# Performance work log

Hardware: AMD Instinct MI355X
Metric: run time of the kernel (lower is better)

## Reference

```python
import jax, jax.numpy as jnp
import numpy as np

N_NODES = 100000
N_EDGES = 1600000
D_FEAT = 256


def _glorot(key, shape):
    fan_in = shape[0]
    return jax.random.normal(key, shape, jnp.float32) * (1.0 / np.sqrt(fan_in))


def setup_inputs() -> dict:
    key = jax.random.key(0)
    ks = jax.random.split(key, 8)
    return {
        "x": jax.random.normal(ks[0], (N_NODES, D_FEAT), jnp.float32),
        "edge_index": jax.random.randint(ks[1], (2, N_EDGES), 0, N_NODES, jnp.int32),
        "w1": _glorot(ks[2], (D_FEAT, 64)),
        "b1": jnp.zeros((64,), jnp.float32),
        "w2": _glorot(ks[3], (64, 32)),
        "b2": jnp.zeros((32,), jnp.float32),
        "wf1": _glorot(ks[4], (32, 16)),
        "bf1": jnp.zeros((16,), jnp.float32),
        "wf2": _glorot(ks[5], (16, 1)),
        "bf2": jnp.zeros((1,), jnp.float32),
    }


def reference(x, edge_index, w1, b1, w2, b2, wf1, bf1, wf2, bf2):
    n = x.shape[0]
    # GCNConv: add self-loops, symmetric D^{-1/2}(A+I)D^{-1/2} normalization
    loops = jnp.arange(n, dtype=edge_index.dtype)
    src = jnp.concatenate([edge_index[0], loops])  # message sources
    dst = jnp.concatenate([edge_index[1], loops])  # aggregation targets
    deg = jax.ops.segment_sum(jnp.ones_like(dst, x.dtype), dst, num_segments=n)
    dinv = jnp.where(deg > 0, jax.lax.rsqrt(jnp.maximum(deg, 1.0)), 0.0)
    norm = dinv[src] * dinv[dst]  # [E+N]

    def gcn_conv(h, W, b):
        hw = h @ W                                   # dense transform first (smaller msg dim)
        msg = hw[src] * norm[:, None]                # gather + scale
        return jax.ops.segment_sum(msg, dst, num_segments=n) + b  # scatter-add

    h = jax.nn.relu(gcn_conv(x, w1, b1))
    h = jax.nn.relu(gcn_conv(h, w2, b2))
    h = jax.nn.relu(h @ wf1 + bf1)
    out = h @ wf2 + bf2
    return out.squeeze(-1)  # [N]
```

## Files before the change

kernel.cpp:

```cpp
#include <hip/hip_runtime.h>
#include <cstdint>
#include <cstddef>

#define N_NODES 100000
#define N_EDGES 1600000

#define NBK   391
#define NPB   256
#define EPB   ((N_EDGES + NPB - 1) / NPB)
#define NSLOT (NBK * NPB)
#define NSB   ((NSLOT + 1023) / 1024)
#define ES_CAP (N_EDGES + NBK * 2048 + 64)

typedef __attribute__((ext_vector_type(8))) short bf16x8;
typedef __attribute__((ext_vector_type(4))) float f32x4;

__device__ __forceinline__ float b2f(unsigned short u) {
    return __uint_as_float(((unsigned)u) << 16);
}
__device__ __forceinline__ unsigned short f2b(float f) {
    unsigned x = __float_as_uint(f);
    return (unsigned short)((x + 0x7FFFu + ((x >> 16) & 1u)) >> 16);
}

__device__ __forceinline__ void split8a(const float* f, bf16x8& hi, bf16x8& lo) {
#pragma unroll
    for (int j = 0; j < 8; ++j) {
        unsigned u = __float_as_uint(f[j]);
        hi[j] = (short)(u >> 16);
        float l = f[j] - __uint_as_float(u & 0xFFFF0000u);
        lo[j] = (short)(__float_as_uint(l) >> 16);
    }
}
__device__ __forceinline__ void split8(const float4& a0, const float4& a1,
                                       bf16x8& hi, bf16x8& lo) {
    float f[8] = {a0.x, a0.y, a0.z, a0.w, a1.x, a1.y, a1.z, a1.w};
    split8a(f, hi, lo);
}


__global__ __launch_bounds__(256) void k_hist(const int* __restrict__ dst,
                                              int* __restrict__ gcnt,
                                              unsigned short* __restrict__ hwb1,
                                              unsigned short* __restrict__ hwb2, int E) {
    __shared__ int lh[NBK];
    int t = threadIdx.x, bid = blockIdx.x;
    if (bid == 0) {
        if (t < 64) hwb1[(size_t)N_NODES * 64 + t] = 0;
        else if (t < 96) hwb2[(size_t)N_NODES * 32 + (t - 64)] = 0;
    }
    for (int i = t; i < NBK; i += 256) lh[i] = 0;
    __syncthreads();
    int e0 = bid * EPB, e1 = min(E, e0 + EPB);
    for (int e = e0 + t; e < e1; e += 256) atomicAdd(&lh[dst[e] >> 8], 1);
    __syncthreads();
    for (int b = t; b < NBK; b += 256) gcnt[b * NPB + bid] = lh[b];
}

__global__ __launch_bounds__(1024) void k_scanA(int* __restrict__ g,
                                                int* __restrict__ bsum, int ntot) {
    __shared__ int s[1024];
    int t = threadIdx.x;
    int i = blockIdx.x * 1024 + t;
    int v = (i < ntot) ? g[i] : 0;
    s[t] = v;
    __syncthreads();
    for (int o = 1; o < 1024; o <<= 1) {
        int a = (t >= o) ? s[t - o] : 0;
        __syncthreads();
        s[t] += a;
        __syncthreads();
    }
    if (i < ntot) g[i] = s[t] - v;
    if (t == 1023) bsum[blockIdx.x] = s[1023];
}

__global__ __launch_bounds__(1024) void k_scanC(int* __restrict__ g,
                                                const int* __restrict__ bsum, int ntot) {
    __shared__ int sp[1024];
    int t = threadIdx.x;
    sp[t] = (t < blockIdx.x && t < NSB) ? bsum[t] : 0;
    __syncthreads();
    for (int o = 512; o > 0; o >>= 1) {
        if (t < o) sp[t] += sp[t + o];
        __syncthreads();
    }
    int pref = sp[0];
    int i = blockIdx.x * 1024 + t;
    if (i < ntot) g[i] += pref;
}

__global__ __launch_bounds__(256) void k_partition(const int* __restrict__ src,
                                                   const int* __restrict__ dst,
                                                   const int* __restrict__ base,
                                                   unsigned* __restrict__ ebuf, int E) {
    __shared__ int lcur[NBK];
    int t = threadIdx.x, bid = blockIdx.x;
    for (int b = t; b < NBK; b += 256) lcur[b] = base[b * NPB + bid];
    __syncthreads();
    int e0 = bid * EPB, e1 = min(E, e0 + EPB);
    for (int e = e0 + t; e < e1; e += 256) {
        int d = dst[e];
        int b = d >> 8;
        int p = atomicAdd(&lcur[b], 1);
        ebuf[p] = (unsigned)src[e] | ((unsigned)(d & 255) << 20);
    }
}

__global__ __launch_bounds__(256) void k_bucket_csr(const int* __restrict__ base,
                                                    const unsigned* __restrict__ ebuf,
                                                    int* __restrict__ cnt,
                                                    float* __restrict__ dinv,
                                                    int* __restrict__ off,
                                                    int* __restrict__ es, int n) {
    __shared__ int lc[256];
    __shared__ int ss[256];
    __shared__ int lo[256];
    __shared__ int lcur[256];
    int b = blockIdx.x, t = threadIdx.x;
    int rstart = base[b * NPB];
    int rend = (b == NBK - 1) ? N_EDGES : base[(b + 1) * NPB];
    int wstart = ((rstart + 7) & ~7) + b * 2048;
    lc[t] = 0;
    __syncthreads();
    for (int e = rstart + t; e < rend; e += 256) atomicAdd(&lc[(int)(ebuf[e] >> 20)], 1);
    __syncthreads();
    int v = lc[t];
    int vp = (v + 7) & ~7;
    ss[t] = vp;
    __syncthreads();
    for (int o = 1; o < 256; o <<= 1) {
        int a = (t >= o) ? ss[t - o] : 0;
        __syncthreads();
        ss[t] += a;
        __syncthreads();
    }
    lo[t] = ss[t] - vp;
    lcur[t] = 0;
    int node = b * 256 + t;
    if (node < n) {
        cnt[node] = vp;
        dinv[node] = rsqrtf((float)v + 1.0f);
        off[node] = wstart + lo[t];
    }
    __syncthreads();
    for (int e = rstart + t; e < rend; e += 256) {
        unsigned u = ebuf[e];
        int l = (int)(u >> 20);
        int p = atomicAdd(&lcur[l], 1);
        es[wstart + lo[l] + p] = (int)(u & 0xFFFFFu);
    }
    for (int q = v; q < vp; ++q) es[wstart + lo[t] + q] = N_NODES;
}


__global__ __launch_bounds__(256) void k_gemm1_mfma(const float* __restrict__ x,
                                                    const float* __restrict__ w,
                                                    const float* __restrict__ dinv,
                                                    unsigned short* __restrict__ out, int M) {
    __shared__ unsigned short Bhi[32 * 64 * 8];
    __shared__ unsigned short Blo[32 * 64 * 8];
    int t = threadIdx.x;
    int wave = t >> 6, lane = t & 63;

    {
        int c = t & 63;
        int kg0 = t >> 6;
#pragma unroll
        for (int i = 0; i < 8; ++i) {
            int kgrp = kg0 + i * 4;
            bf16x8 h8, l8;
#pragma unroll
            for (int j = 0; j < 8; ++j) {
                float f = w[(size_t)(kgrp * 8 + j) * 64 + c];
                unsigned u = __float_as_uint(f);
                h8[j] = (short)(u >> 16);
                float l = f - __uint_as_float(u & 0xFFFF0000u);
                l8[j] = (short)(__float_as_uint(l) >> 16);
            }
            *(bf16x8*)&Bhi[(kgrp * 64 + c) * 8] = h8;
            *(bf16x8*)&Blo[(kgrp * 64 + c) * 8] = l8;
        }
    }
    __syncthreads();

    int row0w = blockIdx.x * 64 + wave * 16;
    int r = row0w + (lane & 15); if (r >= M) r = M - 1;
    const float* xr = x + (size_t)r * 256 + (lane >> 4) * 8;

    f32x4 acc[4] = {{0.f,0.f,0.f,0.f},{0.f,0.f,0.f,0.f},{0.f,0.f,0.f,0.f},{0.f,0.f,0.f,0.f}};

#pragma unroll
    for (int kf = 0; kf < 8; ++kf) {
        float4 a0 = *(const float4*)(xr + kf * 32);
        float4 a1 = *(const float4*)(xr + kf * 32 + 4);
        bf16x8 ahi, alo;
        split8(a0, a1, ahi, alo);
        int kgrpR = kf * 4 + (lane >> 4);
#pragma unroll
        for (int cf = 0; cf < 4; ++cf) {
            bf16x8 bhi = *(const bf16x8*)&Bhi[(kgrpR * 64 + cf * 16 + (lane & 15)) * 8];
            bf16x8 blo = *(const bf16x8*)&Blo[(kgrpR * 64 + cf * 16 + (lane & 15)) * 8];
            acc[cf] = __builtin_amdgcn_mfma_f32_16x16x32_bf16(ahi, bhi, acc[cf], 0, 0, 0);
            acc[cf] = __builtin_amdgcn_mfma_f32_16x16x32_bf16(ahi, blo, acc[cf], 0, 0, 0);
            acc[cf] = __builtin_amdgcn_mfma_f32_16x16x32_bf16(alo, bhi, acc[cf], 0, 0, 0);
        }
    }

#pragma unroll
    for (int j = 0; j < 4; ++j) {
        int rr = row0w + (lane >> 4) * 4 + j;
        if (rr < M) {
            float s = dinv[rr];
#pragma unroll
            for (int cf = 0; cf < 4; ++cf)
                out[(size_t)rr * 64 + cf * 16 + (lane & 15)] = f2b(acc[cf][j] * s);
        }
    }
}


__global__ __launch_bounds__(256) void k_agg1_gemm2(const unsigned short* __restrict__ hwb,
                                                    const float* __restrict__ dinv,
                                                    const int* __restrict__ cnt,
                                                    const int* __restrict__ off,
                                                    const int* __restrict__ es,
                                                    const float* __restrict__ bias,
                                                    const float* __restrict__ w2,
                                                    unsigned short* __restrict__ out) {
    __shared__ float hs[16][68];
    int t = threadIdx.x;
    int wv = t >> 6, lane = t & 63;
    int node0 = blockIdx.x * 16;
    float bl = bias[lane];

#pragma unroll
    for (int i = 0; i < 4; ++i) {
        int node = node0 + wv * 4 + i;
        float dn = dinv[node];
        float acc0 = b2f(hwb[(size_t)node * 64 + lane]);
        float acc1 = 0.0f;
        const int* ep = es + off[node];
        int mp = cnt[node];
        for (int j = 0; j < mp; j += 8) {
            int4 e0 = *(const int4*)&ep[j];
            int4 e1 = *(const int4*)&ep[j + 4];
            float v0 = b2f(hwb[(size_t)e0.x * 64 + lane]);
            float v1 = b2f(hwb[(size_t)e0.y * 64 + lane]);
            float v2 = b2f(hwb[(size_t)e0.z * 64 + lane]);
            float v3 = b2f(hwb[(size_t)e0.w * 64 + lane]);
            float v4 = b2f(hwb[(size_t)e1.x * 64 + lane]);
            float v5 = b2f(hwb[(size_t)e1.y * 64 + lane]);
            float v6 = b2f(hwb[(size_t)e1.z * 64 + lane]);
            float v7 = b2f(hwb[(size_t)e1.w * 64 + lane]);
            acc0 += (v0 + v1) + (v2 + v3);
            acc1 += (v4 + v5) + (v6 + v7);
        }
        hs[wv * 4 + i][lane] = fmaxf(fmaf(dn, acc0 + acc1, bl), 0.0f);
    }
    __syncthreads();

    if (wv < 2) {
        int colbase = wv * 16;
        int r = lane & 15;
        int kg = lane >> 4;
        f32x4 acc = {0.f, 0.f, 0.f, 0.f};
#pragma unroll
        for (int ks = 0; ks < 2; ++ks) {
            float a[8], b[8];
#pragma unroll
            for (int j = 0; j < 8; ++j) {
                int k = ks * 32 + kg * 8 + j;
                a[j] = hs[r][k];
                b[j] = w2[(size_t)k * 32 + colbase + r];
            }
            bf16x8 ahi, alo, bhi, blo;
            split8a(a, ahi, alo);
            split8a(b, bhi, blo);
            acc = __builtin_amdgcn_mfma_f32_16x16x32_bf16(ahi, bhi, acc, 0, 0, 0);
            acc = __builtin_amdgcn_mfma_f32_16x16x32_bf16(ahi, blo, acc, 0, 0, 0);
            acc = __builtin_amdgcn_mfma_f32_16x16x32_bf16(alo, bhi, acc, 0, 0, 0);
        }
#pragma unroll
        for (int reg = 0; reg < 4; ++reg) {
            int row = kg * 4 + reg;
            int nd = node0 + row;
            out[(size_t)nd * 32 + colbase + r] = f2b(acc[reg] * dinv[nd]);
        }
    }
}


__global__ __launch_bounds__(256) void k_agg2_mlp(const unsigned short* __restrict__ hwb,
                                                  const float* __restrict__ dinv,
                                                  const int* __restrict__ cnt,
                                                  const int* __restrict__ off,
                                                  const int* __restrict__ es,
                                                  const float* __restrict__ bias2,
                                                  const float* __restrict__ wf1,
                                                  const float* __restrict__ bf1,
                                                  const float* __restrict__ wf2,
                                                  const float* __restrict__ bf2,
                                                  float* __restrict__ out) {
    __shared__ float hs[8][33];
    __shared__ float W1[512];
    __shared__ float B1[16];
    __shared__ float W2[16];
    int t = threadIdx.x;
    W1[t] = wf1[t];
    W1[t + 256] = wf1[t + 256];
    if (t < 16) { B1[t] = bf1[t]; W2[t] = wf2[t]; }

    int node0 = blockIdx.x * 8;
    int nl = t >> 5;
    int c = t & 31;
    int node = node0 + nl;
    float dn = dinv[node];
    float acc0 = b2f(hwb[(size_t)node * 32 + c]);
    float acc1 = 0.0f;
    const int* ep = es + off[node];
    int mp = cnt[node];
    for (int j = 0; j < mp; j += 8) {
        int4 e0 = *(const int4*)&ep[j];
        int4 e1 = *(const int4*)&ep[j + 4];
        float v0 = b2f(hwb[(size_t)e0.x * 32 + c]);
        float v1 = b2f(hwb[(size_t)e0.y * 32 + c]);
        float v2 = b2f(hwb[(size_t)e0.z * 32 + c]);
        float v3 = b2f(hwb[(size_t)e0.w * 32 + c]);
        float v4 = b2f(hwb[(size_t)e1.x * 32 + c]);
        float v5 = b2f(hwb[(size_t)e1.y * 32 + c]);
        float v6 = b2f(hwb[(size_t)e1.z * 32 + c]);
        float v7 = b2f(hwb[(size_t)e1.w * 32 + c]);
        acc0 += (v0 + v1) + (v2 + v3);
        acc1 += (v4 + v5) + (v6 + v7);
    }
    hs[nl][c] = fmaxf(fmaf(dn, acc0 + acc1, bias2[c]), 0.0f);
    __syncthreads();
    if (t < 128) {
        int nn = t >> 4, jj = t & 15;
        float s = B1[jj];
#pragma unroll
        for (int k = 0; k < 32; ++k) s += hs[nn][k] * W1[k * 16 + jj];
        float p = fmaxf(s, 0.0f) * W2[jj];
        p += __shfl_xor(p, 1);
        p += __shfl_xor(p, 2);
        p += __shfl_xor(p, 4);
        p += __shfl_xor(p, 8);
        if (jj == 0) out[node0 + nn] = p + bf2[0];
    }
}


extern "C" void kernel_launch(void* const* d_in, const int* in_sizes, int n_in,
                              void* d_out, int out_size, void* d_ws, size_t ws_size,
                              hipStream_t stream) {
    const float* x   = (const float*)d_in[0];
    const int*   ei  = (const int*)d_in[1];
    const float* w1  = (const float*)d_in[2];
    const float* b1  = (const float*)d_in[3];
    const float* w2  = (const float*)d_in[4];
    const float* b2  = (const float*)d_in[5];
    const float* wf1 = (const float*)d_in[6];
    const float* bf1 = (const float*)d_in[7];
    const float* wf2 = (const float*)d_in[8];
    const float* bf2 = (const float*)d_in[9];

    const int n = N_NODES;
    const int E = N_EDGES;
    const int* srcp = ei;
    const int* dstp = ei + E;

    char* p = (char*)d_ws;
    auto take = [&](size_t bytes) {
        char* r = p;
        p += (bytes + 255) & ~(size_t)255;
        return r;
    };
    float* dinv = (float*)take((size_t)n * 4);
    int*   cnt  = (int*)take((size_t)n * 4);
    int*   off  = (int*)take((size_t)n * 4);
    int*   gcnt = (int*)take((size_t)NSLOT * 4);
    int*   bsum = (int*)take(512);
    int*   es   = (int*)take((size_t)ES_CAP * 4);
    unsigned short* hwb1 = (unsigned short*)take((size_t)(n + 1) * 64 * 2);
    unsigned short* hwb2 = (unsigned short*)take((size_t)(n + 1) * 32 * 2);
    unsigned* ebuf = (unsigned*)hwb1;

    k_hist<<<NPB, 256, 0, stream>>>(dstp, gcnt, hwb1, hwb2, E);
    k_scanA<<<NSB, 1024, 0, stream>>>(gcnt, bsum, NSLOT);
    k_scanC<<<NSB, 1024, 0, stream>>>(gcnt, bsum, NSLOT);
    k_partition<<<NPB, 256, 0, stream>>>(srcp, dstp, gcnt, ebuf, E);
    k_bucket_csr<<<NBK, 256, 0, stream>>>(gcnt, ebuf, cnt, dinv, off, es, n);

    k_gemm1_mfma<<<(n + 63) / 64, 256, 0, stream>>>(x, w1, dinv, hwb1, n);
    k_agg1_gemm2<<<n / 16, 256, 0, stream>>>(hwb1, dinv, cnt, off, es, b1, w2, hwb2);
    k_agg2_mlp<<<n / 8, 256, 0, stream>>>(hwb2, dinv, cnt, off, es, b2,
                                          wf1, bf1, wf2, bf2, (float*)d_out);
}
```

Baseline: 164.2 us.

## Fold block-sum scan into consumers, stage bucket edges in LDS, interleave node gathers

Removes the k_scanC launch. k_partition and k_bucket_csr now each recompute the 128-entry block-sum prefix and add it to the partially scanned slot counts. k_bucket_csr copies its bucket's packed edges into a shared buffer once and reads them from there in both passes, falling back to global memory past the buffer capacity. k_agg1_gemm2 interleaves the neighbour gathers of the four nodes per wave so more independent loads are in flight. The costs are a redundant small scan in every block, about 20KB of extra LDS, and more live registers in the aggregation loop. The unused bsum_prefix helper is left dead.

```diff
diff --git a/kernel.cpp b/kernel.cpp
--- a/kernel.cpp
+++ b/kernel.cpp
@@ -11,6 +11,7 @@
 #define NSLOT (NBK * NPB)
 #define NSB   ((NSLOT + 1023) / 1024)
 #define ES_CAP (N_EDGES + NBK * 2048 + 64)
+#define EB_CAP 5120
 
 typedef __attribute__((ext_vector_type(8))) short bf16x8;
 typedef __attribute__((ext_vector_type(4))) float f32x4;
@@ -75,28 +76,54 @@
     if (t == 1023) bsum[blockIdx.x] = s[1023];
 }
 
-__global__ __launch_bounds__(1024) void k_scanC(int* __restrict__ g,
-                                                const int* __restrict__ bsum, int ntot) {
-    __shared__ int sp[1024];
+__device__ __forceinline__ void bsum_prefix(const int* __restrict__ bsum, int* pe) {
     int t = threadIdx.x;
-    sp[t] = (t < blockIdx.x && t < NSB) ? bsum[t] : 0;
-    __syncthreads();
-    for (int o = 512; o > 0; o >>= 1) {
-        if (t < o) sp[t] += sp[t + o];
-        __syncthreads();
-    }
-    int pref = sp[0];
-    int i = blockIdx.x * 1024 + t;
-    if (i < ntot) g[i] += pref;
+    if (t < 128) {
+        int v = (t < NSB) ? bsum[t] : 0;
+        pe[t] = v;
+    }
+    __syncthreads();
+    if (t < 128) {
+        int v = pe[t];
+        int acc = v;
+#pragma unroll
+        for (int o = 1; o < 128; o <<= 1) {
+            int a = (t >= o) ? pe[t - o] : 0;
+            __syncthreads();
+            if (t < 128) pe[t] = acc = acc + a;
+            __syncthreads();
+        }
+        pe[t] = acc - v;
+    }
+    __syncthreads();
 }
 
 __global__ __launch_bounds__(256) void k_partition(const int* __restrict__ src,
                                                    const int* __restrict__ dst,
-                                                   const int* __restrict__ base,
+                                                   const int* __restrict__ g,
+                                                   const int* __restrict__ bsum,
                                                    unsigned* __restrict__ ebuf, int E) {
     __shared__ int lcur[NBK];
+    __shared__ int pe[128];
     int t = threadIdx.x, bid = blockIdx.x;
-    for (int b = t; b < NBK; b += 256) lcur[b] = base[b * NPB + bid];
+    {
+        int v = 0;
+        if (t < 128) { v = (t < NSB) ? bsum[t] : 0; pe[t] = v; }
+        __syncthreads();
+        for (int o = 1; o < 128; o <<= 1) {
+            int a = 0;
+            if (t < 128 && t >= o) a = pe[t - o];
+            __syncthreads();
+            if (t < 128) pe[t] += a;
+            __syncthreads();
+        }
+        if (t < 128) pe[t] -= v;
+        __syncthreads();
+    }
+    for (int b = t; b < NBK; b += 256) {
+        int slot = b * NPB + bid;
+        lcur[b] = g[slot] + pe[slot >> 10];
+    }
     __syncthreads();
     int e0 = bid * EPB, e1 = min(E, e0 + EPB);
     for (int e = e0 + t; e < e1; e += 256) {
@@ -107,23 +134,49 @@
     }
 }
 
-__global__ __launch_bounds__(256) void k_bucket_csr(const int* __restrict__ base,
+__global__ __launch_bounds__(256) void k_bucket_csr(const int* __restrict__ g,
+                                                    const int* __restrict__ bsum,
                                                     const unsigned* __restrict__ ebuf,
                                                     int* __restrict__ cnt,
                                                     float* __restrict__ dinv,
                                                     int* __restrict__ off,
                                                     int* __restrict__ es, int n) {
+    __shared__ unsigned eb[EB_CAP];
     __shared__ int lc[256];
     __shared__ int ss[256];
     __shared__ int lo[256];
     __shared__ int lcur[256];
+    __shared__ int pe[128];
     int b = blockIdx.x, t = threadIdx.x;
-    int rstart = base[b * NPB];
-    int rend = (b == NBK - 1) ? N_EDGES : base[(b + 1) * NPB];
+    {
+        int v = 0;
+        if (t < 128) { v = (t < NSB) ? bsum[t] : 0; pe[t] = v; }
+        __syncthreads();
+        for (int o = 1; o < 128; o <<= 1) {
+            int a = 0;
+            if (t < 128 && t >= o) a = pe[t - o];
+            __syncthreads();
+            if (t < 128) pe[t] += a;
+            __syncthreads();
+        }
+        if (t < 128) pe[t] -= v;
+        __syncthreads();
+    }
+    int s0 = b * NPB;
+    int rstart = g[s0] + pe[s0 >> 10];
+    int rend;
+    if (b == NBK - 1) rend = N_EDGES;
+    else { int s1 = (b + 1) * NPB; rend = g[s1] + pe[s1 >> 10]; }
+    int m = rend - rstart;
+    int ms = min(m, EB_CAP);
     int wstart = ((rstart + 7) & ~7) + b * 2048;
     lc[t] = 0;
-    __syncthreads();
-    for (int e = rstart + t; e < rend; e += 256) atomicAdd(&lc[(int)(ebuf[e] >> 20)], 1);
+    for (int i = t; i < ms; i += 256) eb[i] = ebuf[rstart + i];
+    __syncthreads();
+    for (int e = t; e < m; e += 256) {
+        unsigned u = (e < ms) ? eb[e] : ebuf[rstart + e];
+        atomicAdd(&lc[(int)(u >> 20)], 1);
+    }
     __syncthreads();
     int v = lc[t];
     int vp = (v + 7) & ~7;
@@ -144,8 +197,8 @@
         off[node] = wstart + lo[t];
     }
     __syncthreads();
-    for (int e = rstart + t; e < rend; e += 256) {
-        unsigned u = ebuf[e];
+    for (int e = t; e < m; e += 256) {
+        unsigned u = (e < ms) ? eb[e] : ebuf[rstart + e];
         int l = (int)(u >> 20);
         int p = atomicAdd(&lcur[l], 1);
         es[wstart + lo[l] + p] = (int)(u & 0xFFFFFu);
@@ -234,30 +287,41 @@
     int node0 = blockIdx.x * 16;
     float bl = bias[lane];
 
+    float dn[4], a0[4], a1[4];
+    const int* ep[4];
+    int mp[4];
 #pragma unroll
     for (int i = 0; i < 4; ++i) {
         int node = node0 + wv * 4 + i;
-        float dn = dinv[node];
-        float acc0 = b2f(hwb[(size_t)node * 64 + lane]);
-        float acc1 = 0.0f;
-        const int* ep = es + off[node];
-        int mp = cnt[node];
-        for (int j = 0; j < mp; j += 8) {
-            int4 e0 = *(const int4*)&ep[j];
-            int4 e1 = *(const int4*)&ep[j + 4];
-            float v0 = b2f(hwb[(size_t)e0.x * 64 + lane]);
-            float v1 = b2f(hwb[(size_t)e0.y * 64 + lane]);
-            float v2 = b2f(hwb[(size_t)e0.z * 64 + lane]);
-            float v3 = b2f(hwb[(size_t)e0.w * 64 + lane]);
-            float v4 = b2f(hwb[(size_t)e1.x * 64 + lane]);
-            float v5 = b2f(hwb[(size_t)e1.y * 64 + lane]);
-            float v6 = b2f(hwb[(size_t)e1.z * 64 + lane]);
-            float v7 = b2f(hwb[(size_t)e1.w * 64 + lane]);
-            acc0 += (v0 + v1) + (v2 + v3);
-            acc1 += (v4 + v5) + (v6 + v7);
-        }
-        hs[wv * 4 + i][lane] = fmaxf(fmaf(dn, acc0 + acc1, bl), 0.0f);
-    }
+        dn[i] = dinv[node];
+        a0[i] = b2f(hwb[(size_t)node * 64 + lane]);
+        a1[i] = 0.0f;
+        ep[i] = es + off[node];
+        mp[i] = cnt[node];
+    }
+    int mmax = max(max(mp[0], mp[1]), max(mp[2], mp[3]));
+    for (int j = 0; j < mmax; j += 8) {
+#pragma unroll
+        for (int i = 0; i < 4; ++i) {
+            if (j < mp[i]) {
+                int4 e0 = *(const int4*)&ep[i][j];
+                int4 e1 = *(const int4*)&ep[i][j + 4];
+                float v0 = b2f(hwb[(size_t)e0.x * 64 + lane]);
+                float v1 = b2f(hwb[(size_t)e0.y * 64 + lane]);
+                float v2 = b2f(hwb[(size_t)e0.z * 64 + lane]);
+                float v3 = b2f(hwb[(size_t)e0.w * 64 + lane]);
+                float v4 = b2f(hwb[(size_t)e1.x * 64 + lane]);
+                float v5 = b2f(hwb[(size_t)e1.y * 64 + lane]);
+                float v6 = b2f(hwb[(size_t)e1.z * 64 + lane]);
+                float v7 = b2f(hwb[(size_t)e1.w * 64 + lane]);
+                a0[i] += (v0 + v1) + (v2 + v3);
+                a1[i] += (v4 + v5) + (v6 + v7);
+            }
+        }
+    }
+#pragma unroll
+    for (int i = 0; i < 4; ++i)
+        hs[wv * 4 + i][lane] = fmaxf(fmaf(dn[i], a0[i] + a1[i], bl), 0.0f);
     __syncthreads();
 
     if (wv < 2) {
@@ -388,9 +452,8 @@
 
     k_hist<<<NPB, 256, 0, stream>>>(dstp, gcnt, hwb1, hwb2, E);
     k_scanA<<<NSB, 1024, 0, stream>>>(gcnt, bsum, NSLOT);
-    k_scanC<<<NSB, 1024, 0, stream>>>(gcnt, bsum, NSLOT);
-    k_partition<<<NPB, 256, 0, stream>>>(srcp, dstp, gcnt, ebuf, E);
-    k_bucket_csr<<<NBK, 256, 0, stream>>>(gcnt, ebuf, cnt, dinv, off, es, n);
+    k_partition<<<NPB, 256, 0, stream>>>(srcp, dstp, gcnt, bsum, ebuf, E);
+    k_bucket_csr<<<NBK, 256, 0, stream>>>(gcnt, bsum, ebuf, cnt, dinv, off, es, n);
 
     k_gemm1_mfma<<<(n + 63) / 64, 256, 0, stream>>>(x, w1, dinv, hwb1, n);
     k_agg1_gemm2<<<n / 16, 256, 0, stream>>>(hwb1, dinv, cnt, off, es, b1, w2, hwb2);
```

New measurement: 161.1 us. About the same (-1.9%).
